# Optimization experiments

Hardware: AMD Instinct MI355X
Metric: run time of the kernel (lower is better)

## Reference

```python
import jax, jax.numpy as jnp
import numpy as np

N_HEAD = 12
HEAD_DIM = 64
N_EMBD = 768
ATTN_MULT = 0.125
B, T = 2, 2048
NEG_INF = -1e30


def setup_inputs() -> dict:
    key = jax.random.key(0)
    ks = jax.random.split(key, 3)
    x = jax.random.normal(ks[0], (B, T, N_EMBD), dtype=jnp.float32)
    W_attn = jax.random.normal(ks[1], (N_EMBD, 3 * N_HEAD * HEAD_DIM), dtype=jnp.float32) * 0.02
    b_attn = jnp.zeros((3 * N_HEAD * HEAD_DIM,), dtype=jnp.float32)
    W_proj = jax.random.normal(ks[2], (N_HEAD * HEAD_DIM, N_EMBD), dtype=jnp.float32) * 0.02
    b_proj = jnp.zeros((N_EMBD,), dtype=jnp.float32)
    return {"x": x, "W_attn": W_attn, "b_attn": b_attn, "W_proj": W_proj, "b_proj": b_proj}


def reference(x, W_attn, b_attn, W_proj, b_proj):
    Bsz, Tlen, C = x.shape
    H, D = N_HEAD, HEAD_DIM
    qkv = x @ W_attn + b_attn                       # [B,T,3*H*D]
    q, k, v = jnp.split(qkv, 3, axis=-1)
    q = q.reshape(Bsz, Tlen, H, D).transpose(0, 2, 1, 3)   # [B,H,T,D]
    k = k.reshape(Bsz, Tlen, H, D).transpose(0, 2, 1, 3)
    v = v.reshape(Bsz, Tlen, H, D).transpose(0, 2, 1, 3)

    att = jnp.einsum('bhtd,bhsd->bhts', q, k) * ATTN_MULT  # [B,H,T,T]
    causal = jnp.tril(jnp.ones((Tlen, Tlen), dtype=bool))  # [T,T]
    att = jnp.where(causal, att, NEG_INF)

    # selection mask from head 0 (SelectionHeadLinearComboKind.NONE)
    S = jax.nn.relu(att[:, 0:1, :, :])                     # [B,1,T,T]; relu kills -inf
    # protect_bos_token: zero column 0 (key index 0)
    col = jnp.arange(Tlen)
    S = S * (col[None, None, None, :] != 0)
    # prevent_from_masking_myself: zero diagonal
    S = S * (1.0 - jnp.eye(Tlen, dtype=S.dtype))

    # accumulate selection over query (row) axis: ProtectionKind.NONE
    FF = jnp.cumsum(S, axis=-2)                            # [B,1,T,T]
    att = att - FF                                         # broadcast over heads

    p = jax.nn.softmax(att, axis=-1)                       # [B,H,T,T]
    y = jnp.einsum('bhts,bhsd->bhtd', p, v)                # [B,H,T,D]
    y = y.transpose(0, 2, 1, 3).reshape(Bsz, Tlen, H * D)  # [B,T,H*D]
    return y @ W_proj + b_proj
```

## Files before the change

kernel.cpp:

```cpp
#include <hip/hip_runtime.h>
#include <math.h>

#define T 2048
#define NH 12
#define HD 64
#define C3 2304
#define CE 768
#define NB 2

typedef __attribute__((ext_vector_type(8))) short bf16x8;
typedef __attribute__((ext_vector_type(4))) float f32x4;

__device__ inline void bf16split(float a, unsigned short& h, unsigned short& l) {
    unsigned int u = __float_as_uint(a);
    unsigned int r = (u + 0x7FFFu + ((u >> 16) & 1u)) >> 16;
    h = (unsigned short)r;
    float hf = __uint_as_float(r << 16);
    float lo = a - hf;
    unsigned int v = __float_as_uint(lo);
    l = (unsigned short)((v + 0x7FFFu + ((v >> 16) & 1u)) >> 16);
}

__global__ __launch_bounds__(256) void cvt_split_kernel(const float* __restrict__ A,
        unsigned short* __restrict__ H, unsigned short* __restrict__ L) {
    int i = blockIdx.x * 256 + threadIdx.x;
    float4 a0 = *(reinterpret_cast<const float4*>(A) + (size_t)i * 2);
    float4 a1 = *(reinterpret_cast<const float4*>(A) + (size_t)i * 2 + 1);
    float f[8] = {a0.x, a0.y, a0.z, a0.w, a1.x, a1.y, a1.z, a1.w};
    unsigned short h[8], l[8];
    #pragma unroll
    for (int j = 0; j < 8; ++j) bf16split(f[j], h[j], l[j]);
    uint4 hv, lv;
    hv.x = (unsigned)h[0] | ((unsigned)h[1] << 16); hv.y = (unsigned)h[2] | ((unsigned)h[3] << 16);
    hv.z = (unsigned)h[4] | ((unsigned)h[5] << 16); hv.w = (unsigned)h[6] | ((unsigned)h[7] << 16);
    lv.x = (unsigned)l[0] | ((unsigned)l[1] << 16); lv.y = (unsigned)l[2] | ((unsigned)l[3] << 16);
    lv.z = (unsigned)l[4] | ((unsigned)l[5] << 16); lv.w = (unsigned)l[6] | ((unsigned)l[7] << 16);
    reinterpret_cast<uint4*>(H)[i] = hv;
    reinterpret_cast<uint4*>(L)[i] = lv;
}

__global__ __launch_bounds__(256) void cvt_split_T_kernel(const float* __restrict__ W,
        unsigned short* __restrict__ H, unsigned short* __restrict__ L, int K, int N) {
    __shared__ float tile[64][65];
    const int n0 = blockIdx.x * 64, k0 = blockIdx.y * 64;
    const int t = threadIdx.x;
    {
        int r = t >> 2, c4 = (t & 3) * 16;
        #pragma unroll
        for (int u = 0; u < 4; ++u) {
            float4 w = *reinterpret_cast<const float4*>(&W[(size_t)(k0 + r) * N + n0 + c4 + u * 4]);
            tile[r][c4 + u * 4 + 0] = w.x; tile[r][c4 + u * 4 + 1] = w.y;
            tile[r][c4 + u * 4 + 2] = w.z; tile[r][c4 + u * 4 + 3] = w.w;
        }
    }
    __syncthreads();
    {
        int n = t >> 2, kc = (t & 3) * 16;
        unsigned short h[16], l[16];
        #pragma unroll
        for (int j = 0; j < 16; ++j) bf16split(tile[kc + j][n], h[j], l[j]);
        uint4 hv0, hv1, lv0, lv1;
        hv0.x = (unsigned)h[0] | ((unsigned)h[1] << 16);  hv0.y = (unsigned)h[2] | ((unsigned)h[3] << 16);
        hv0.z = (unsigned)h[4] | ((unsigned)h[5] << 16);  hv0.w = (unsigned)h[6] | ((unsigned)h[7] << 16);
        hv1.x = (unsigned)h[8] | ((unsigned)h[9] << 16);  hv1.y = (unsigned)h[10] | ((unsigned)h[11] << 16);
        hv1.z = (unsigned)h[12] | ((unsigned)h[13] << 16); hv1.w = (unsigned)h[14] | ((unsigned)h[15] << 16);
        lv0.x = (unsigned)l[0] | ((unsigned)l[1] << 16);  lv0.y = (unsigned)l[2] | ((unsigned)l[3] << 16);
        lv0.z = (unsigned)l[4] | ((unsigned)l[5] << 16);  lv0.w = (unsigned)l[6] | ((unsigned)l[7] << 16);
        lv1.x = (unsigned)l[8] | ((unsigned)l[9] << 16);  lv1.y = (unsigned)l[10] | ((unsigned)l[11] << 16);
        lv1.z = (unsigned)l[12] | ((unsigned)l[13] << 16); lv1.w = (unsigned)l[14] | ((unsigned)l[15] << 16);
        size_t o = (size_t)(n0 + n) * K + k0 + kc;
        reinterpret_cast<uint4*>(&H[o])[0] = hv0; reinterpret_cast<uint4*>(&H[o])[1] = hv1;
        reinterpret_cast<uint4*>(&L[o])[0] = lv0; reinterpret_cast<uint4*>(&L[o])[1] = lv1;
    }
}

__global__ __launch_bounds__(256) void cvt_qk_kernel(const float* __restrict__ qkv,
        unsigned short* __restrict__ Qh, unsigned short* __restrict__ Ql,
        unsigned short* __restrict__ Kh, unsigned short* __restrict__ Kl) {
    int t = blockIdx.x * 256 + threadIdx.x;
    int dg = t & 7;
    int s = (t >> 3) & (T - 1);
    int bh = t >> 14;
    int b = bh / NH, h = bh % NH;
    const float* qs = qkv + (size_t)(b * T + s) * C3 + h * 64 + dg * 8;
    const float* ks = qs + 768;
    size_t o = ((size_t)bh * T + s) * 64 + dg * 8;
    #pragma unroll
    for (int which = 0; which < 2; ++which) {
        const float* src = (which == 0) ? qs : ks;
        float4 a0 = *reinterpret_cast<const float4*>(src);
        float4 a1 = *reinterpret_cast<const float4*>(src + 4);
        float f[8] = {a0.x, a0.y, a0.z, a0.w, a1.x, a1.y, a1.z, a1.w};
        unsigned short hh[8], ll[8];
        #pragma unroll
        for (int j = 0; j < 8; ++j) bf16split(f[j], hh[j], ll[j]);
        uint4 hv, lv;
        hv.x = (unsigned)hh[0] | ((unsigned)hh[1] << 16); hv.y = (unsigned)hh[2] | ((unsigned)hh[3] << 16);
        hv.z = (unsigned)hh[4] | ((unsigned)hh[5] << 16); hv.w = (unsigned)hh[6] | ((unsigned)hh[7] << 16);
        lv.x = (unsigned)ll[0] | ((unsigned)ll[1] << 16); lv.y = (unsigned)ll[2] | ((unsigned)ll[3] << 16);
        lv.z = (unsigned)ll[4] | ((unsigned)ll[5] << 16); lv.w = (unsigned)ll[6] | ((unsigned)ll[7] << 16);
        if (which == 0) {
            *reinterpret_cast<uint4*>(&Qh[o]) = hv;
            *reinterpret_cast<uint4*>(&Ql[o]) = lv;
// ... 245 lines not shown
        }
        return;
    }
    __shared__ float Qt[64][68];
    __shared__ float Kt[64][68];
    {
        int r = tid >> 2;
        int c0 = (tid & 3) * 16;
        const float* qrow = qkv + (size_t)(b * T + qb + r) * C3 + 0;
        const float* krow = qkv + (size_t)(b * T + kb + r) * C3 + 768;
        #pragma unroll
        for (int u = 0; u < 4; ++u) {
            float4 q4 = *reinterpret_cast<const float4*>(&qrow[c0 + u * 4]);
            float4 k4 = *reinterpret_cast<const float4*>(&krow[c0 + u * 4]);
            int d = c0 + u * 4;
            Qt[d + 0][r] = q4.x; Qt[d + 1][r] = q4.y; Qt[d + 2][r] = q4.z; Qt[d + 3][r] = q4.w;
            Kt[d + 0][r] = k4.x; Kt[d + 1][r] = k4.y; Kt[d + 2][r] = k4.z; Kt[d + 3][r] = k4.w;
        }
    }
    __syncthreads();
    float acc[4][4] = {};
    #pragma unroll
    for (int d = 0; d < 64; ++d) {
        float4 qv = *reinterpret_cast<const float4*>(&Qt[d][ty * 4]);
        float4 kv = *reinterpret_cast<const float4*>(&Kt[d][tx * 4]);
        float qa[4] = {qv.x, qv.y, qv.z, qv.w};
        float ka[4] = {kv.x, kv.y, kv.z, kv.w};
        #pragma unroll
        for (int i = 0; i < 4; ++i)
            #pragma unroll
            for (int j = 0; j < 4; ++j)
                acc[i][j] = fmaf(qa[i], ka[j], acc[i][j]);
    }
    #pragma unroll
    for (int i = 0; i < 4; ++i) {
        int t = qb + ty * 4 + i;
        float o[4];
        #pragma unroll
        for (int j = 0; j < 4; ++j) {
            int s = kb + tx * 4 + j;
            float v = acc[i][j] * 0.125f;
            o[j] = (s >= 1 && s < t) ? fmaxf(v, 0.0f) : 0.0f;
        }
        float4 o4 = {o[0], o[1], o[2], o[3]};
        *reinterpret_cast<float4*>(&Sb[(size_t)t * T + kb + tx * 4]) = o4;
    }
}

__global__ __launch_bounds__(256) void colsum_kernel(const float* __restrict__ S,
                                                     float* __restrict__ Psum) {
    int s = blockIdx.x * 256 + threadIdx.x;
    int j = blockIdx.y, b = blockIdx.z;
    const float* Sb = S + (size_t)b * T * T;
    float sum = 0.f;
    for (int r = 0; r < 64; ++r) sum += Sb[(size_t)(j * 64 + r) * T + s];
    Psum[((size_t)b * 32 + j) * T + s] = sum;
}

__global__ __launch_bounds__(256) void scanseg_kernel(float* __restrict__ Psum) {
    int s = blockIdx.x * 256 + threadIdx.x;
    int b = blockIdx.y;
    float run = 0.f;
    for (int j = 0; j < 32; ++j) {
        size_t idx = ((size_t)b * 32 + j) * T + s;
        float v = Psum[idx];
        Psum[idx] = run;
        run += v;
    }
}

__global__ __launch_bounds__(256) void ffscan_kernel(float* __restrict__ S,
                                                     const float* __restrict__ Psum) {
    int s = blockIdx.x * 256 + threadIdx.x;
    int j = blockIdx.y, b = blockIdx.z;
    float run = Psum[((size_t)b * 32 + j) * T + s];
    float* Sb = S + (size_t)b * T * T;
    for (int r = 0; r < 64; ++r) {
        size_t idx = (size_t)(j * 64 + r) * T + s;
        run += Sb[idx];
        Sb[idx] = run;
    }
}

__device__ inline int chunk_base_fn(int qt) {
    int base = 0;
    for (int q = 8; q < qt; ++q) base += (q + 8) >> 3;
    return base;
}

__global__ __launch_bounds__(256) void flash_mfma_kernel(
        const unsigned short* __restrict__ Qh, const unsigned short* __restrict__ Ql,
        const unsigned short* __restrict__ Kh, const unsigned short* __restrict__ Kl,
        const unsigned short* __restrict__ Vth, const unsigned short* __restrict__ Vtl,
        const float* __restrict__ FF, float* __restrict__ Y,
        float* __restrict__ PART) {
    const int hb = blockIdx.x;
    const int h = hb % NH, b = hb / NH;
    int qt = 0, kt0 = 0, kt1 = 1;
    {
        int u = blockIdx.y, cnt = 0;
        bool found = false;
        for (int sz = 8; sz >= 1 && !found; --sz) {
            for (int q = 31; q >= 0; --q) {
                int nch = (q + 8) >> 3;
                int nfull = nch - 1;
                int last = q + 1 - 8 * nfull;
                int nthis = ((sz == 8) ? nfull : 0) + ((last == sz) ? 1 : 0);
                if (u < cnt + nthis) {
                    int off = u - cnt;
                    qt = q;
                    int ci = (sz == 8 && off < nfull) ? off : nfull;
                    kt0 = ci * 8;
                    kt1 = (ci == nfull) ? (q + 1) : (kt0 + 8);
                    found = true;
                    break;
                }
                cnt += nthis;
            }
        }
    }
    const int qb = qt * 64;
    const int tid = threadIdx.x;
    const int lane = tid & 63, w = tid >> 6;
    const int fr = lane & 15, fg = lane >> 4;
    __shared__ unsigned short KP[2][64 * FST];
    __shared__ unsigned short Vt[2][64 * FST];

    bf16x8 qh[2], ql[2];
    #pragma unroll
    for (int ks = 0; ks < 2; ++ks) {
        size_t qo = ((size_t)hb * T + qb + w * 16 + fr) * 64 + ks * 32 + fg * 8;
        qh[ks] = *reinterpret_cast<const bf16x8*>(&Qh[qo]);
        ql[ks] = *reinterpret_cast<const bf16x8*>(&Ql[qo]);
    }

    float m[4], l[4];
    f32x4 Oacc[4];
    #pragma unroll
    for (int p = 0; p < 4; ++p) { m[p] = -1e30f; l[p] = 0.f; }
    #pragma unroll
    for (int fd = 0; fd < 4; ++fd) Oacc[fd] = (f32x4){0.f, 0.f, 0.f, 0.f};

    const float* FFb = FF + (size_t)b * T * T;
    const int sr = tid >> 2, sc0 = (tid & 3) * 16;

    for (int kt = kt0; kt < kt1; ++kt) {
        const int kb = kt * 64;
        __syncthreads();
        {
            const unsigned short* ksrc = Kh + ((size_t)hb * T + kb + sr) * 64 + sc0;
            const unsigned short* ksrl = Kl + ((size_t)hb * T + kb + sr) * 64 + sc0;
            const unsigned short* vsrc = Vth + ((size_t)hb * 64 + sr) * T + kb + sc0;
            const unsigned short* vsrl = Vtl + ((size_t)hb * 64 + sr) * T + kb + sc0;
            uint4 k0v = reinterpret_cast<const uint4*>(ksrc)[0];
            uint4 k1v = reinterpret_cast<const uint4*>(ksrc)[1];
            uint4 k2v = reinterpret_cast<const uint4*>(ksrl)[0];
            uint4 k3v = reinterpret_cast<const uint4*>(ksrl)[1];
            uint4 v0v = reinterpret_cast<const uint4*>(vsrc)[0];
            uint4 v1v = reinterpret_cast<const uint4*>(vsrc)[1];
            uint4 v2v = reinterpret_cast<const uint4*>(vsrl)[0];
            uint4 v3v = reinterpret_cast<const uint4*>(vsrl)[1];
            *reinterpret_cast<uint4*>(&KP[0][sr * FST + sc0 + 0]) = k0v;
            *reinterpret_cast<uint4*>(&KP[0][sr * FST + sc0 + 8]) = k1v;
            *reinterpret_cast<uint4*>(&KP[1][sr * FST + sc0 + 0]) = k2v;
            *reinterpret_cast<uint4*>(&KP[1][sr * FST + sc0 + 8]) = k3v;
            *reinterpret_cast<uint4*>(&Vt[0][sr * FST + sc0 + 0]) = v0v;
            *reinterpret_cast<uint4*>(&Vt[0][sr * FST + sc0 + 8]) = v1v;
            *reinterpret_cast<uint4*>(&Vt[1][sr * FST + sc0 + 0]) = v2v;
            *reinterpret_cast<uint4*>(&Vt[1][sr * FST + sc0 + 8]) = v3v;
        }
        __syncthreads();
        float ffv[4][4];
        #pragma unroll
        for (int p = 0; p < 4; ++p) {
            int t = qb + w * 16 + fg * 4 + p;
            #pragma unroll
            for (int fj = 0; fj < 4; ++fj)
                ffv[p][fj] = FFb[(size_t)t * T + kb + fj * 16 + fr];
        }
        f32x4 qk[4];
        #pragma unroll
        for (int fj = 0; fj < 4; ++fj) qk[fj] = (f32x4){0.f, 0.f, 0.f, 0.f};
        #pragma unroll
        for (int ks = 0; ks < 2; ++ks) {
            bf16x8 kbh[4], kbl[4];
            #pragma unroll
            for (int fj = 0; fj < 4; ++fj) {
                kbh[fj] = *reinterpret_cast<const bf16x8*>(&KP[0][(fj * 16 + fr) * FST + ks * 32 + fg * 8]);
                kbl[fj] = *reinterpret_cast<const bf16x8*>(&KP[1][(fj * 16 + fr) * FST + ks * 32 + fg * 8]);
            }
            #pragma unroll
            for (int fj = 0; fj < 4; ++fj) {
                qk[fj] = __builtin_amdgcn_mfma_f32_16x16x32_bf16(qh[ks], kbh[fj], qk[fj], 0, 0, 0);
                qk[fj] = __builtin_amdgcn_mfma_f32_16x16x32_bf16(qh[ks], kbl[fj], qk[fj], 0, 0, 0);
                qk[fj] = __builtin_amdgcn_mfma_f32_16x16x32_bf16(ql[ks], kbh[fj], qk[fj], 0, 0, 0);
            }
        }
        float sc[4][4];
        #pragma unroll
        for (int p = 0; p < 4; ++p) {
            int t = qb + w * 16 + fg * 4 + p;
            #pragma unroll
            for (int fj = 0; fj < 4; ++fj) {
                int s = kb + fj * 16 + fr;
                float v = qk[fj][p] * 0.125f - ffv[p][fj];
                sc[fj][p] = (s <= t) ? v : -1e30f;
            }
        }
        #pragma unroll
        for (int p = 0; p < 4; ++p) {
            float tm = fmaxf(fmaxf(sc[0][p], sc[1][p]), fmaxf(sc[2][p], sc[3][p]));
            tm = fmaxf(tm, __shfl_xor(tm, 1));
            tm = fmaxf(tm, __shfl_xor(tm, 2));
            tm = fmaxf(tm, __shfl_xor(tm, 4));
            tm = fmaxf(tm, __shfl_xor(tm, 8));
            float mn = fmaxf(m[p], tm);
            float scale = __expf(m[p] - mn);
            float rs = 0.f;
            #pragma unroll
            for (int fj = 0; fj < 4; ++fj) {
                float pe = __expf(sc[fj][p] - mn);
                sc[fj][p] = pe; rs += pe;
            }
            rs += __shfl_xor(rs, 1); rs += __shfl_xor(rs, 2);
            rs += __shfl_xor(rs, 4); rs += __shfl_xor(rs, 8);
            l[p] = l[p] * scale + rs;
            m[p] = mn;
            #pragma unroll
            for (int fd = 0; fd < 4; ++fd) Oacc[fd][p] *= scale;
        }
        __syncthreads();
        #pragma unroll
        for (int p = 0; p < 4; ++p) {
            int qrow = w * 16 + fg * 4 + p;
            #pragma unroll
            for (int fj = 0; fj < 4; ++fj) {
                unsigned short hh, ll;
                bf16split(sc[fj][p], hh, ll);
                KP[0][qrow * FST + fj * 16 + fr] = hh;
                KP[1][qrow * FST + fj * 16 + fr] = ll;
            }
        }
        __syncthreads();
        #pragma unroll
        for (int ks = 0; ks < 2; ++ks) {
            bf16x8 pah = *reinterpret_cast<const bf16x8*>(&KP[0][(w * 16 + fr) * FST + ks * 32 + fg * 8]);
            bf16x8 pal = *reinterpret_cast<const bf16x8*>(&KP[1][(w * 16 + fr) * FST + ks * 32 + fg * 8]);
            bf16x8 vbh[4], vbl[4];
            #pragma unroll
            for (int fd = 0; fd < 4; ++fd) {
                vbh[fd] = *reinterpret_cast<const bf16x8*>(&Vt[0][(fd * 16 + fr) * FST + ks * 32 + fg * 8]);
                vbl[fd] = *reinterpret_cast<const bf16x8*>(&Vt[1][(fd * 16 + fr) * FST + ks * 32 + fg * 8]);
            }
            #pragma unroll
            for (int fd = 0; fd < 4; ++fd) {
                Oacc[fd] = __builtin_amdgcn_mfma_f32_16x16x32_bf16(pah, vbh[fd], Oacc[fd], 0, 0, 0);
                Oacc[fd] = __builtin_amdgcn_mfma_f32_16x16x32_bf16(pah, vbl[fd], Oacc[fd], 0, 0, 0);
                Oacc[fd] = __builtin_amdgcn_mfma_f32_16x16x32_bf16(pal, vbh[fd], Oacc[fd], 0, 0, 0);
            }
        }
    }
    if (qt < 8) {
        #pragma unroll
        for (int p = 0; p < 4; ++p) {
            int t = qb + w * 16 + fg * 4 + p;
            float inv = 1.f / l[p];
            float* Yrow = Y + (size_t)(b * T + t) * CE + h * 64;
            #pragma unroll
            for (int fd = 0; fd < 4; ++fd)
                Yrow[fd * 16 + fr] = Oacc[fd][p] * inv;
        }
    } else {
        const int cb = chunk_base_fn(qt) + (kt0 >> 3);
        float* Ob = PART + (size_t)(hb * 72 + cb) * 4224;
        #pragma unroll
        for (int p = 0; p < 4; ++p) {
            int rr = w * 16 + fg * 4 + p;
            #pragma unroll
            for (int fd = 0; fd < 4; ++fd)
                Ob[rr * 64 + fd * 16 + fr] = Oacc[fd][p];
            if (fr == 0) { Ob[4096 + rr] = m[p]; Ob[4096 + 64 + rr] = l[p]; }
        }
    }
}

__global__ __launch_bounds__(256) void merge8_kernel(const float* __restrict__ PART,
                                                     float* __restrict__ Y) {
    const int hb = blockIdx.x;
    const int qt = 8 + blockIdx.y;
    const int h = hb % NH, b = hb / NH;
    const int nch = (qt + 8) >> 3;
    const float* base = PART + (size_t)(hb * 72 + chunk_base_fn(qt)) * 4224;
    const int tid = threadIdx.x;
    const int r = tid >> 2, c0 = (tid & 3) * 16;
    float mm[4], ll[4];
    float M = -1e30f;
    #pragma unroll
    for (int c = 0; c < 4; ++c) {
        int cc = (c < nch) ? c : 0;
        float mv = base[(size_t)cc * 4224 + 4096 + r];
        float lv = base[(size_t)cc * 4224 + 4096 + 64 + r];
        mm[c] = (c < nch) ? mv : -1e30f;
        ll[c] = (c < nch) ? lv : 0.f;
        M = fmaxf(M, mm[c]);
    }
    float a[4], L = 0.f;
    #pragma unroll
    for (int c = 0; c < 4; ++c) {
        a[c] = (c < nch) ? __expf(mm[c] - M) : 0.f;
        L += a[c] * ll[c];
    }
    float inv = 1.f / L;
    const int t = qt * 64 + r;
    float* Yrow = Y + (size_t)(b * T + t) * CE + h * 64;
    #pragma unroll
    for (int u = 0; u < 4; ++u) {
        float ax = 0.f, ay = 0.f, az = 0.f, aw = 0.f;
        #pragma unroll
        for (int c = 0; c < 4; ++c) {
            int cc = (c < nch) ? c : 0;
            float4 xo = *reinterpret_cast<const float4*>(&base[(size_t)cc * 4224 + r * 64 + c0 + u * 4]);
            ax += a[c] * xo.x; ay += a[c] * xo.y; az += a[c] * xo.z; aw += a[c] * xo.w;
        }
        float4 y = {ax * inv, ay * inv, az * inv, aw * inv};
        *reinterpret_cast<float4*>(&Yrow[c0 + u * 4]) = y;
    }
}

__global__ __launch_bounds__(256) void flash_kernel(const float* __restrict__ qkv,
                                                    const float* __restrict__ FF,
                                                    float* __restrict__ Y,
                                                    float* __restrict__ PO,
                                                    float* __restrict__ PML,
                                                    int split) {
    const int hb = blockIdx.x;
    const int h = hb % NH, b = hb / NH;
    int qt, kt0, kt1, mode;
    if (split) {
        const int u = blockIdx.y;
        if (u < 16)      { qt = 16 + u; kt0 = 0;  kt1 = 16;     mode = 1; }
        else if (u < 32) { qt = 31 - u; kt0 = 0;  kt1 = qt + 1; mode = 0; }
        else             { qt = 63 - u; kt0 = 16; kt1 = qt + 1; mode = 2; }
    } else {
        qt = 31 - blockIdx.y; kt0 = 0; kt1 = qt + 1; mode = 0;
    }
    const int qb = qt * 64;
    const int tid = threadIdx.x, ty = tid >> 4, tx = tid & 15;
    __shared__ float Qt[64][68];
    __shared__ float KtPs[64][68];
    __shared__ float Vs[64][68];
    const int r = tid >> 2, c0 = (tid & 3) * 16;
    {
        const float* qrow = qkv + (size_t)(b * T + qb + r) * C3 + h * 64;
        #pragma unroll
        for (int u = 0; u < 4; ++u) {
            float4 q4 = *reinterpret_cast<const float4*>(&qrow[c0 + u * 4]);
            int d = c0 + u * 4;
            Qt[d + 0][r] = q4.x; Qt[d + 1][r] = q4.y; Qt[d + 2][r] = q4.z; Qt[d + 3][r] = q4.w;
        }
    }
    float m[4], l[4], O[4][4];
    #pragma unroll
    for (int i = 0; i < 4; ++i) {
        m[i] = -1e30f; l[i] = 0.f;
        #pragma unroll
        for (int j = 0; j < 4; ++j) O[i][j] = 0.f;
    }
    const float* FFb = FF + (size_t)b * T * T;
    for (int kt = kt0; kt < kt1; ++kt) {
        const int kb = kt * 64;
        __syncthreads();
        {
            const float* krow = qkv + (size_t)(b * T + kb + r) * C3 + 768 + h * 64;
            const float* vrow = qkv + (size_t)(b * T + kb + r) * C3 + 1536 + h * 64;
            #pragma unroll
            for (int u = 0; u < 4; ++u) {
                float4 k4 = *reinterpret_cast<const float4*>(&krow[c0 + u * 4]);
                int d = c0 + u * 4;
                KtPs[d + 0][r] = k4.x; KtPs[d + 1][r] = k4.y;
                KtPs[d + 2][r] = k4.z; KtPs[d + 3][r] = k4.w;
                *reinterpret_cast<float4*>(&Vs[r][c0 + u * 4]) =
                    *reinterpret_cast<const float4*>(&vrow[c0 + u * 4]);
            }
        }
        __syncthreads();
        float sc[4][4] = {};
        #pragma unroll
        for (int d = 0; d < 64; ++d) {
            float4 qv = *reinterpret_cast<const float4*>(&Qt[d][ty * 4]);
            float4 kv = *reinterpret_cast<const float4*>(&KtPs[d][tx * 4]);
            float qa[4] = {qv.x, qv.y, qv.z, qv.w};
            float ka[4] = {kv.x, kv.y, kv.z, kv.w};
            #pragma unroll
            for (int i = 0; i < 4; ++i)
                #pragma unroll
                for (int j = 0; j < 4; ++j)
                    sc[i][j] = fmaf(qa[i], ka[j], sc[i][j]);
        }
        #pragma unroll
        for (int i = 0; i < 4; ++i) {
            int t = qb + ty * 4 + i;
            float4 f4 = *reinterpret_cast<const float4*>(&FFb[(size_t)t * T + kb + tx * 4]);
            float fv[4] = {f4.x, f4.y, f4.z, f4.w};
            #pragma unroll
            for (int j = 0; j < 4; ++j) {
                int s = kb + tx * 4 + j;
                float v = sc[i][j] * 0.125f - fv[j];
                sc[i][j] = (s <= t) ? v : -1e30f;
            }
        }
        #pragma unroll
        for (int i = 0; i < 4; ++i) {
            float tm = fmaxf(fmaxf(sc[i][0], sc[i][1]), fmaxf(sc[i][2], sc[i][3]));
            tm = fmaxf(tm, __shfl_xor(tm, 1));
            tm = fmaxf(tm, __shfl_xor(tm, 2));
            tm = fmaxf(tm, __shfl_xor(tm, 4));
            tm = fmaxf(tm, __shfl_xor(tm, 8));
            float mn = fmaxf(m[i], tm);
            float scale = __expf(m[i] - mn);
            float rs = 0.f;
            #pragma unroll
            for (int j = 0; j < 4; ++j) {
                float p = __expf(sc[i][j] - mn);
                sc[i][j] = p; rs += p;
            }
            rs += __shfl_xor(rs, 1); rs += __shfl_xor(rs, 2);
            rs += __shfl_xor(rs, 4); rs += __shfl_xor(rs, 8);
            l[i] = l[i] * scale + rs;
            m[i] = mn;
            #pragma unroll
            for (int j = 0; j < 4; ++j) O[i][j] *= scale;
        }
        __syncthreads();
        #pragma unroll
        for (int i = 0; i < 4; ++i) {
            float4 p4 = {sc[i][0], sc[i][1], sc[i][2], sc[i][3]};
            *reinterpret_cast<float4*>(&KtPs[ty * 4 + i][tx * 4]) = p4;
        }
        __syncthreads();
        #pragma unroll
        for (int j4 = 0; j4 < 16; ++j4) {
            float pv[4][4];
            #pragma unroll
            for (int i = 0; i < 4; ++i) {
                float4 t4 = *reinterpret_cast<const float4*>(&KtPs[ty * 4 + i][j4 * 4]);
                pv[i][0] = t4.x; pv[i][1] = t4.y; pv[i][2] = t4.z; pv[i][3] = t4.w;
            }
            #pragma unroll
            for (int jj = 0; jj < 4; ++jj) {
                float4 v4 = *reinterpret_cast<const float4*>(&Vs[j4 * 4 + jj][tx * 4]);
                float vv[4] = {v4.x, v4.y, v4.z, v4.w};
                #pragma unroll
                for (int i = 0; i < 4; ++i)
                    #pragma unroll
                    for (int dd = 0; dd < 4; ++dd)
                        O[i][dd] = fmaf(pv[i][jj], vv[dd], O[i][dd]);
            }
        }
    }
    if (mode == 0) {
        #pragma unroll
        for (int i = 0; i < 4; ++i) {
            int t = qb + ty * 4 + i;
            float inv = 1.f / l[i];
            float4 o4 = {O[i][0] * inv, O[i][1] * inv, O[i][2] * inv, O[i][3] * inv};
            *reinterpret_cast<float4*>(&Y[(size_t)(b * T + t) * CE + h * 64 + tx * 4]) = o4;
        }
    } else {
        const int pidx = (b * NH + h) * 16 + (qt - 16);
        float* Ob  = PO  + (size_t)(mode - 1) * (NB * NH * 16 * 4096) + (size_t)pidx * 4096;
        float* mlb = PML + (size_t)(mode - 1) * (NB * NH * 16 * 128)  + (size_t)pidx * 128;
        #pragma unroll
        for (int i = 0; i < 4; ++i) {
            int rr = ty * 4 + i;
            float4 o4 = {O[i][0], O[i][1], O[i][2], O[i][3]};
            *reinterpret_cast<float4*>(&Ob[rr * 64 + tx * 4]) = o4;
            if (tx == 0) { mlb[rr] = m[i]; mlb[64 + rr] = l[i]; }
        }
    }
}

__global__ __launch_bounds__(256) void merge_kernel(const float* __restrict__ PO,
                                                    const float* __restrict__ PML,
                                                    float* __restrict__ Y) {
    const int p = blockIdx.x;
    const int q16 = p & 15;
    const int hb = p >> 4;
    const int h = hb % NH, b = hb / NH;
    const int qt = 16 + q16;
    const float* O0  = PO  + (size_t)p * 4096;
    const float* O1  = PO  + (size_t)(NB * NH * 16) * 4096 + (size_t)p * 4096;
    const float* ml0 = PML + (size_t)p * 128;
    const float* ml1 = PML + (size_t)(NB * NH * 16) * 128  + (size_t)p * 128;
    const int tid = threadIdx.x;
    const int r = tid >> 2, c0 = (tid & 3) * 16;
    float m0 = ml0[r], l0 = ml0[64 + r];
    float m1 = ml1[r], l1 = ml1[64 + r];
    float M  = fmaxf(m0, m1);
    float a0 = __expf(m0 - M), a1 = __expf(m1 - M);
    float inv = 1.f / (a0 * l0 + a1 * l1);
    const int t = qt * 64 + r;
    float* Yrow = Y + (size_t)(b * T + t) * CE + h * 64;
    #pragma unroll
    for (int u = 0; u < 4; ++u) {
        float4 x0 = *reinterpret_cast<const float4*>(&O0[r * 64 + c0 + u * 4]);
        float4 x1 = *reinterpret_cast<const float4*>(&O1[r * 64 + c0 + u * 4]);
        float4 y;
        y.x = (a0 * x0.x + a1 * x1.x) * inv;
        y.y = (a0 * x0.y + a1 * x1.y) * inv;
        y.z = (a0 * x0.z + a1 * x1.z) * inv;
        y.w = (a0 * x0.w + a1 * x1.w) * inv;
        *reinterpret_cast<float4*>(&Yrow[c0 + u * 4]) = y;
    }
}

extern "C" void kernel_launch(void* const* d_in, const int* in_sizes, int n_in,
                              void* d_out, int out_size, void* d_ws, size_t ws_size,
                              hipStream_t stream) {
    const float* x      = (const float*)d_in[0];
    const float* W_attn = (const float*)d_in[1];
    const float* b_attn = (const float*)d_in[2];
    const float* W_proj = (const float*)d_in[3];
    const float* b_proj = (const float*)d_in[4];
    float* out = (float*)d_out;

    char* ws = (char*)d_ws;
    const size_t QKV_BYTES = (size_t)NB * T * C3 * 4;
    const size_t S_BYTES   = (size_t)NB * T * T * 4;
    const size_t P_BYTES   = (size_t)NB * 32 * T * 4;
    const size_t Y_BYTES   = (size_t)NB * T * CE * 4;
    const size_t PO_BYTES  = (size_t)2 * NB * NH * 16 * 4096 * 4;
    const size_t PML_BYTES = (size_t)2 * NB * NH * 16 * 128 * 4;
    const size_t PLANE_X   = (size_t)NB * T * CE * 2;
    const size_t PLANE_WA  = (size_t)C3 * CE * 2;
    const size_t PLANE_WP  = (size_t)CE * CE * 2;
    const size_t PLANE_KV  = (size_t)NB * NH * T * 64 * 2;

    const size_t U_OFF  = QKV_BYTES + S_BYTES + P_BYTES + Y_BYTES;
    const size_t U_SIZE = PO_BYTES + PML_BYTES;
    const size_t W_OFF  = U_OFF + U_SIZE;
    const size_t KV_OFF = W_OFF + 2 * PLANE_WA + 2 * PLANE_WP;

    float* qkv  = (float*)ws;
    float* S    = (float*)(ws + QKV_BYTES);
    float* Psum = (float*)(ws + QKV_BYTES + S_BYTES);
    float* Yb   = (float*)(ws + QKV_BYTES + S_BYTES + P_BYTES);
    float* PO   = (float*)(ws + U_OFF);
    float* PML  = (float*)(ws + U_OFF + PO_BYTES);
    unsigned short* Xh  = (unsigned short*)(ws + U_OFF);
    unsigned short* Xl  = (unsigned short*)(ws + U_OFF + PLANE_X);
    unsigned short* Qhp = Xh;
    unsigned short* Qlp = Xl;
    unsigned short* Yh  = Xh;
    unsigned short* Yl  = Xl;
    unsigned short* WAh = (unsigned short*)(ws + W_OFF);
    unsigned short* WAl = (unsigned short*)(ws + W_OFF + PLANE_WA);
    unsigned short* WPh = (unsigned short*)(ws + W_OFF + 2 * PLANE_WA);
    unsigned short* WPl = (unsigned short*)(ws + W_OFF + 2 * PLANE_WA + PLANE_WP);
    unsigned short* Khp = (unsigned short*)(ws + KV_OFF);
    unsigned short* Klp = (unsigned short*)(ws + KV_OFF + PLANE_KV);
    unsigned short* VTh = (unsigned short*)(ws + KV_OFF + 2 * PLANE_KV);
    unsigned short* VTl = (unsigned short*)(ws + KV_OFF + 3 * PLANE_KV);
    float* PART = qkv;

    const size_t NEED_SPLIT = U_OFF + U_SIZE;
    const size_t NEED_MFMA  = KV_OFF;
    const size_t NEED_KV    = KV_OFF + 4 * PLANE_KV;
    const int split = (ws_size >= NEED_SPLIT) ? 1 : 0;
    const int mfma  = (ws_size >= NEED_MFMA) ? 1 : 0;
    const int kv    = (ws_size >= NEED_KV && mfma) ? 1 : 0;

    const int M = NB * T;

    if (mfma) {
        cvt_split_T_kernel<<<dim3(C3 / 64, CE / 64), 256, 0, stream>>>(W_attn, WAh, WAl, CE, C3);
        cvt_split_T_kernel<<<dim3(CE / 64, CE / 64), 256, 0, stream>>>(W_proj, WPh, WPl, CE, CE);
        cvt_split_kernel<<<dim3((M * CE / 8) / 256), 256, 0, stream>>>(x, Xh, Xl);
        gemm_mfma_kernel<<<dim3(C3 / 128, M / 128), 256, 0, stream>>>(Xh, Xl, WAh, WAl, b_attn, qkv, M, C3, CE);
    } else {
        gemm_bias_kernel<<<dim3(C3 / 64, M / 64), 256, 0, stream>>>(x, W_attn, b_attn, qkv, M, C3, CE);
    }
    if (kv) {
        cvt_qk_kernel<<<dim3((NB * NH * T * 8) / 256), 256, 0, stream>>>(qkv, Qhp, Qlp, Khp, Klp);
        cvt_kv_vt_kernel<<<dim3(T / 64, NB * NH), 256, 0, stream>>>(qkv, VTh, VTl);
        s0_mfma_kernel<<<dim3(T / 64, T / 64, NB), 256, 0, stream>>>(Qhp, Qlp, Khp, Klp, S);
    } else {
        s0_kernel<<<dim3(T / 64, T / 64, NB), 256, 0, stream>>>(qkv, S);
    }
    colsum_kernel<<<dim3(T / 256, 32, NB), 256, 0, stream>>>(S, Psum);
    scanseg_kernel<<<dim3(T / 256, NB), 256, 0, stream>>>(Psum);
    ffscan_kernel<<<dim3(T / 256, 32, NB), 256, 0, stream>>>(S, Psum);
    if (kv) {
        flash_mfma_kernel<<<dim3(NB * NH, 80), 256, 0, stream>>>(Qhp, Qlp, Khp, Klp, VTh, VTl, S, Yb, PART);
        merge8_kernel<<<dim3(NB * NH, 24), 256, 0, stream>>>(PART, Yb);
    } else if (split) {
        flash_kernel<<<dim3(NB * NH, 48), 256, 0, stream>>>(qkv, S, Yb, PO, PML, 1);
        merge_kernel<<<dim3(NB * NH * 16), 256, 0, stream>>>(PO, PML, Yb);
    } else {
        flash_kernel<<<dim3(NB * NH, 32), 256, 0, stream>>>(qkv, S, Yb, PO, PML, 0);
    }
    if (mfma) {
        cvt_split_kernel<<<dim3((M * CE / 8) / 256), 256, 0, stream>>>(Yb, Yh, Yl);
        gemm_mfma_kernel<<<dim3(CE / 128, M / 128), 256, 0, stream>>>(Yh, Yl, WPh, WPl, b_proj, out, M, CE, CE);
    } else {
        gemm_bias_kernel<<<dim3(CE / 64, M / 64), 256, 0, stream>>>(Yb, W_proj, b_proj, out, M, CE, CE);
    }
}
```

Before: 296.5 us.

## Use 128-row query tiles with 32x32 MFMA and register-resident P in flash kernel

Restructures the flash attention kernel to process 128-query tiles using 32x32x16 bf16 MFMAs, where each wave owns 32 query rows. Scores are computed transposed so the softmax row stats need only a single cross-half shuffle. P is repacked through lane shuffles instead of a round trip through shared memory, which removes two barriers per key tile. Work partitioning moves to precomputed lookup tables with 40 blocks and a matching 128-row merge kernel. Fewer, larger blocks reuse K/V more but may lower occupancy and raise register pressure.

```diff
diff --git a/kernel.cpp b/kernel.cpp
--- a/kernel.cpp
+++ b/kernel.cpp
@@ -10,6 +10,8 @@
 
 typedef __attribute__((ext_vector_type(8))) short bf16x8;
 typedef __attribute__((ext_vector_type(4))) float f32x4;
+typedef __attribute__((ext_vector_type(16))) float f32x16;
+typedef __attribute__((ext_vector_type(4))) unsigned u32x4;
 
 __device__ inline void bf16split(float a, unsigned short& h, unsigned short& l) {
     unsigned int u = __float_as_uint(a);
@@ -19,6 +21,13 @@
     float lo = a - hf;
     unsigned int v = __float_as_uint(lo);
     l = (unsigned short)((v + 0x7FFFu + ((v >> 16) & 1u)) >> 16);
+}
+
+__device__ inline void packP(float a, float b, unsigned& wh, unsigned& wl) {
+    unsigned short ha, la, hb, lb;
+    bf16split(a, ha, la); bf16split(b, hb, lb);
+    wh = (unsigned)ha | ((unsigned)hb << 16);
+    wl = (unsigned)la | ((unsigned)lb << 16);
 }
 
 __global__ __launch_bounds__(256) void cvt_split_kernel(const float* __restrict__ A,
@@ -430,11 +439,10 @@
     }
 }
 
-__device__ inline int chunk_base_fn(int qt) {
-    int base = 0;
-    for (int q = 8; q < qt; ++q) base += (q + 8) >> 3;
-    return base;
-}
+__device__ const int FTQ[40] = {15,15,15,15,14,14,14,13,13,13,12,12,12,11,11,11,10,10,9,9,8,8,7,7,6,5,4,3,14,10,6,2,13,9,5,1,12,8,4,0};
+__device__ const int FK0[40] = {0,8,16,24,0,8,16,0,8,16,0,8,16,0,8,16,0,8,0,8,0,8,0,8,0,0,0,0,24,16,8,0,24,16,8,0,24,16,8,0};
+__device__ const int FK1[40] = {8,16,24,32,8,16,24,8,16,24,8,16,24,8,16,24,8,16,8,16,8,16,8,16,8,8,8,8,30,22,14,6,28,20,12,4,26,18,10,2};
+__device__ const int FCB[12] = {0,2,4,6,8,11,14,17,20,24,28,32};
 
 __global__ __launch_bounds__(256) void flash_mfma_kernel(
         const unsigned short* __restrict__ Qh, const unsigned short* __restrict__ Ql,
@@ -444,51 +452,26 @@
         float* __restrict__ PART) {
     const int hb = blockIdx.x;
     const int h = hb % NH, b = hb / NH;
-    int qt = 0, kt0 = 0, kt1 = 1;
-    {
-        int u = blockIdx.y, cnt = 0;
-        bool found = false;
-        for (int sz = 8; sz >= 1 && !found; --sz) {
-            for (int q = 31; q >= 0; --q) {
-                int nch = (q + 8) >> 3;
-                int nfull = nch - 1;
-                int last = q + 1 - 8 * nfull;
-                int nthis = ((sz == 8) ? nfull : 0) + ((last == sz) ? 1 : 0);
-                if (u < cnt + nthis) {
-                    int off = u - cnt;
-                    qt = q;
-                    int ci = (sz == 8 && off < nfull) ? off : nfull;
-                    kt0 = ci * 8;
-                    kt1 = (ci == nfull) ? (q + 1) : (kt0 + 8);
-                    found = true;
-                    break;
-                }
-                cnt += nthis;
-            }
-        }
-    }
-    const int qb = qt * 64;
+    const int u = blockIdx.y;
+    const int tq = FTQ[u], kt0 = FK0[u], kt1 = FK1[u];
+    const int qb = tq * 128;
     const int tid = threadIdx.x;
     const int lane = tid & 63, w = tid >> 6;
-    const int fr = lane & 15, fg = lane >> 4;
-    __shared__ unsigned short KP[2][64 * FST];
-    __shared__ unsigned short Vt[2][64 * FST];
-
-    bf16x8 qh[2], ql[2];
-    #pragma unroll
-    for (int ks = 0; ks < 2; ++ks) {
-        size_t qo = ((size_t)hb * T + qb + w * 16 + fr) * 64 + ks * 32 + fg * 8;
-        qh[ks] = *reinterpret_cast<const bf16x8*>(&Qh[qo]);
-        ql[ks] = *reinterpret_cast<const bf16x8*>(&Ql[qo]);
-    }
-
-    float m[4], l[4];
-    f32x4 Oacc[4];
-    #pragma unroll
-    for (int p = 0; p < 4; ++p) { m[p] = -1e30f; l[p] = 0.f; }
-    #pragma unroll
-    for (int fd = 0; fd < 4; ++fd) Oacc[fd] = (f32x4){0.f, 0.f, 0.f, 0.f};
-
+    const int q31 = lane & 31, hi = lane >> 5;
+    const int trow = qb + w * 32 + q31;
+    __shared__ unsigned short KS[2][64 * FST];
+    __shared__ unsigned short VS[2][64 * FST];
+
+    bf16x8 qfh[4], qfl[4];
+    #pragma unroll
+    for (int dblk = 0; dblk < 4; ++dblk) {
+        size_t qo = ((size_t)hb * T + trow) * 64 + dblk * 16 + hi * 8;
+        qfh[dblk] = *reinterpret_cast<const bf16x8*>(&Qh[qo]);
+        qfl[dblk] = *reinterpret_cast<const bf16x8*>(&Ql[qo]);
+    }
+
+    f32x16 oacc0 = (f32x16)(0.f), oacc1 = (f32x16)(0.f);
+    float m = -1e30f, l = 0.f;
     const float* FFb = FF + (size_t)b * T * T;
     const int sr = tid >> 2, sc0 = (tid & 3) * 16;
 
@@ -508,170 +491,182 @@
             uint4 v1v = reinterpret_cast<const uint4*>(vsrc)[1];
             uint4 v2v = reinterpret_cast<const uint4*>(vsrl)[0];
             uint4 v3v = reinterpret_cast<const uint4*>(vsrl)[1];
-            *reinterpret_cast<uint4*>(&KP[0][sr * FST + sc0 + 0]) = k0v;
-            *reinterpret_cast<uint4*>(&KP[0][sr * FST + sc0 + 8]) = k1v;
-            *reinterpret_cast<uint4*>(&KP[1][sr * FST + sc0 + 0]) = k2v;
-            *reinterpret_cast<uint4*>(&KP[1][sr * FST + sc0 + 8]) = k3v;
-            *reinterpret_cast<uint4*>(&Vt[0][sr * FST + sc0 + 0]) = v0v;
-            *reinterpret_cast<uint4*>(&Vt[0][sr * FST + sc0 + 8]) = v1v;
-            *reinterpret_cast<uint4*>(&Vt[1][sr * FST + sc0 + 0]) = v2v;
-            *reinterpret_cast<uint4*>(&Vt[1][sr * FST + sc0 + 8]) = v3v;
+            *reinterpret_cast<uint4*>(&KS[0][sr * FST + sc0 + 0]) = k0v;
+            *reinterpret_cast<uint4*>(&KS[0][sr * FST + sc0 + 8]) = k1v;
+            *reinterpret_cast<uint4*>(&KS[1][sr * FST + sc0 + 0]) = k2v;
+            *reinterpret_cast<uint4*>(&KS[1][sr * FST + sc0 + 8]) = k3v;
+            *reinterpret_cast<uint4*>(&VS[0][sr * FST + sc0 + 0]) = v0v;
+            *reinterpret_cast<uint4*>(&VS[0][sr * FST + sc0 + 8]) = v1v;
+            *reinterpret_cast<uint4*>(&VS[1][sr * FST + sc0 + 0]) = v2v;
+            *reinterpret_cast<uint4*>(&VS[1][sr * FST + sc0 + 8]) = v3v;
         }
         __syncthreads();
-        float ffv[4][4];
-        #pragma unroll
-        for (int p = 0; p < 4; ++p) {
-            int t = qb + w * 16 + fg * 4 + p;
-            #pragma unroll
-            for (int fj = 0; fj < 4; ++fj)
-                ffv[p][fj] = FFb[(size_t)t * T + kb + fj * 16 + fr];
-        }
-        f32x4 qk[4];
-        #pragma unroll
-        for (int fj = 0; fj < 4; ++fj) qk[fj] = (f32x4){0.f, 0.f, 0.f, 0.f};
-        #pragma unroll
-        for (int ks = 0; ks < 2; ++ks) {
-            bf16x8 kbh[4], kbl[4];
-            #pragma unroll
-            for (int fj = 0; fj < 4; ++fj) {
-                kbh[fj] = *reinterpret_cast<const bf16x8*>(&KP[0][(fj * 16 + fr) * FST + ks * 32 + fg * 8]);
-                kbl[fj] = *reinterpret_cast<const bf16x8*>(&KP[1][(fj * 16 + fr) * FST + ks * 32 + fg * 8]);
-            }
-            #pragma unroll
-            for (int fj = 0; fj < 4; ++fj) {
-                qk[fj] = __builtin_amdgcn_mfma_f32_16x16x32_bf16(qh[ks], kbh[fj], qk[fj], 0, 0, 0);
-                qk[fj] = __builtin_amdgcn_mfma_f32_16x16x32_bf16(qh[ks], kbl[fj], qk[fj], 0, 0, 0);
-                qk[fj] = __builtin_amdgcn_mfma_f32_16x16x32_bf16(ql[ks], kbh[fj], qk[fj], 0, 0, 0);
-            }
-        }
-        float sc[4][4];
-        #pragma unroll
-        for (int p = 0; p < 4; ++p) {
-            int t = qb + w * 16 + fg * 4 + p;
-            #pragma unroll
-            for (int fj = 0; fj < 4; ++fj) {
-                int s = kb + fj * 16 + fr;
-                float v = qk[fj][p] * 0.125f - ffv[p][fj];
-                sc[fj][p] = (s <= t) ? v : -1e30f;
-            }
-        }
-        #pragma unroll
-        for (int p = 0; p < 4; ++p) {
-            float tm = fmaxf(fmaxf(sc[0][p], sc[1][p]), fmaxf(sc[2][p], sc[3][p]));
-            tm = fmaxf(tm, __shfl_xor(tm, 1));
-            tm = fmaxf(tm, __shfl_xor(tm, 2));
-            tm = fmaxf(tm, __shfl_xor(tm, 4));
-            tm = fmaxf(tm, __shfl_xor(tm, 8));
-            float mn = fmaxf(m[p], tm);
-            float scale = __expf(m[p] - mn);
-            float rs = 0.f;
-            #pragma unroll
-            for (int fj = 0; fj < 4; ++fj) {
-                float pe = __expf(sc[fj][p] - mn);
-                sc[fj][p] = pe; rs += pe;
-            }
-            rs += __shfl_xor(rs, 1); rs += __shfl_xor(rs, 2);
-            rs += __shfl_xor(rs, 4); rs += __shfl_xor(rs, 8);
-            l[p] = l[p] * scale + rs;
-            m[p] = mn;
-            #pragma unroll
-            for (int fd = 0; fd < 4; ++fd) Oacc[fd][p] *= scale;
-        }
-        __syncthreads();
-        #pragma unroll
-        for (int p = 0; p < 4; ++p) {
-            int qrow = w * 16 + fg * 4 + p;
-            #pragma unroll
-            for (int fj = 0; fj < 4; ++fj) {
-                unsigned short hh, ll;
-                bf16split(sc[fj][p], hh, ll);
-                KP[0][qrow * FST + fj * 16 + fr] = hh;
-                KP[1][qrow * FST + fj * 16 + fr] = ll;
-            }
-        }
-        __syncthreads();
-        #pragma unroll
-        for (int ks = 0; ks < 2; ++ks) {
-            bf16x8 pah = *reinterpret_cast<const bf16x8*>(&KP[0][(w * 16 + fr) * FST + ks * 32 + fg * 8]);
-            bf16x8 pal = *reinterpret_cast<const bf16x8*>(&KP[1][(w * 16 + fr) * FST + ks * 32 + fg * 8]);
-            bf16x8 vbh[4], vbl[4];
-            #pragma unroll
-            for (int fd = 0; fd < 4; ++fd) {
-                vbh[fd] = *reinterpret_cast<const bf16x8*>(&Vt[0][(fd * 16 + fr) * FST + ks * 32 + fg * 8]);
-                vbl[fd] = *reinterpret_cast<const bf16x8*>(&Vt[1][(fd * 16 + fr) * FST + ks * 32 + fg * 8]);
-            }
-            #pragma unroll
-            for (int fd = 0; fd < 4; ++fd) {
-                Oacc[fd] = __builtin_amdgcn_mfma_f32_16x16x32_bf16(pah, vbh[fd], Oacc[fd], 0, 0, 0);
-                Oacc[fd] = __builtin_amdgcn_mfma_f32_16x16x32_bf16(pah, vbl[fd], Oacc[fd], 0, 0, 0);
-                Oacc[fd] = __builtin_amdgcn_mfma_f32_16x16x32_bf16(pal, vbh[fd], Oacc[fd], 0, 0, 0);
-            }
-        }
-    }
-    if (qt < 8) {
-        #pragma unroll
-        for (int p = 0; p < 4; ++p) {
-            int t = qb + w * 16 + fg * 4 + p;
-            float inv = 1.f / l[p];
-            float* Yrow = Y + (size_t)(b * T + t) * CE + h * 64;
-            #pragma unroll
-            for (int fd = 0; fd < 4; ++fd)
-                Yrow[fd * 16 + fr] = Oacc[fd][p] * inv;
+        f32x16 acc[2];
+        acc[0] = (f32x16)(0.f); acc[1] = (f32x16)(0.f);
+        #pragma unroll
+        for (int sb = 0; sb < 2; ++sb) {
+            #pragma unroll
+            for (int dblk = 0; dblk < 4; ++dblk) {
+                bf16x8 kfh = *reinterpret_cast<const bf16x8*>(&KS[0][(sb * 32 + q31) * FST + dblk * 16 + hi * 8]);
+                bf16x8 kfl = *reinterpret_cast<const bf16x8*>(&KS[1][(sb * 32 + q31) * FST + dblk * 16 + hi * 8]);
+                acc[sb] = __builtin_amdgcn_mfma_f32_32x32x16_bf16(kfh, qfh[dblk], acc[sb], 0, 0, 0);
+                acc[sb] = __builtin_amdgcn_mfma_f32_32x32x16_bf16(kfh, qfl[dblk], acc[sb], 0, 0, 0);
+                acc[sb] = __builtin_amdgcn_mfma_f32_32x32x16_bf16(kfl, qfh[dblk], acc[sb], 0, 0, 0);
+            }
+        }
+        float pv[2][16];
+        #pragma unroll
+        for (int sb = 0; sb < 2; ++sb) {
+            #pragma unroll
+            for (int g = 0; g < 4; ++g) {
+                float4 f4 = *reinterpret_cast<const float4*>(
+                    &FFb[(size_t)trow * T + kb + sb * 32 + g * 8 + hi * 4]);
+                float fv[4] = {f4.x, f4.y, f4.z, f4.w};
+                #pragma unroll
+                for (int a = 0; a < 4; ++a) {
+                    int r = g * 4 + a;
+                    int s = kb + sb * 32 + a + g * 8 + hi * 4;
+                    float val = acc[sb][r] * 0.125f - fv[a];
+                    pv[sb][r] = (s <= trow) ? val : -1e30f;
+                }
+            }
+        }
+        float tm = pv[0][0];
+        #pragma unroll
+        for (int sb = 0; sb < 2; ++sb)
+            #pragma unroll
+            for (int r = 0; r < 16; ++r) tm = fmaxf(tm, pv[sb][r]);
+        tm = fmaxf(tm, __shfl_xor(tm, 32));
+        float mn = fmaxf(m, tm);
+        float scale = __expf(m - mn);
+        float rs = 0.f;
+        #pragma unroll
+        for (int sb = 0; sb < 2; ++sb)
+            #pragma unroll
+            for (int r = 0; r < 16; ++r) {
+                float pe = __expf(pv[sb][r] - mn);
+                pv[sb][r] = pe; rs += pe;
+            }
+        rs += __shfl_xor(rs, 32);
+        l = l * scale + rs;
+        m = mn;
+        oacc0 *= scale; oacc1 *= scale;
+        unsigned wh[2][4][2], wl[2][4][2];
+        #pragma unroll
+        for (int sb = 0; sb < 2; ++sb)
+            #pragma unroll
+            for (int bq = 0; bq < 4; ++bq)
+                #pragma unroll
+                for (int h2 = 0; h2 < 2; ++h2)
+                    packP(pv[sb][4 * bq + 2 * h2], pv[sb][4 * bq + 2 * h2 + 1],
+                          wh[sb][bq][h2], wl[sb][bq][h2]);
+        #pragma unroll
+        for (int kk = 0; kk < 4; ++kk) {
+            const int sb = kk >> 1;
+            const int b0 = 2 * (kk & 1), b1 = b0 + 1;
+            unsigned sh_b1_0 = (unsigned)__shfl_xor((int)wh[sb][b1][0], 32);
+            unsigned sh_b1_1 = (unsigned)__shfl_xor((int)wh[sb][b1][1], 32);
+            unsigned sh_b0_0 = (unsigned)__shfl_xor((int)wh[sb][b0][0], 32);
+            unsigned sh_b0_1 = (unsigned)__shfl_xor((int)wh[sb][b0][1], 32);
+            unsigned sl_b1_0 = (unsigned)__shfl_xor((int)wl[sb][b1][0], 32);
+            unsigned sl_b1_1 = (unsigned)__shfl_xor((int)wl[sb][b1][1], 32);
+            unsigned sl_b0_0 = (unsigned)__shfl_xor((int)wl[sb][b0][0], 32);
+            unsigned sl_b0_1 = (unsigned)__shfl_xor((int)wl[sb][b0][1], 32);
+            u32x4 th, tl;
+            th[0] = hi ? sh_b1_0 : wh[sb][b0][0];
+            th[1] = hi ? sh_b1_1 : wh[sb][b0][1];
+            th[2] = hi ? wh[sb][b1][0] : sh_b0_0;
+            th[3] = hi ? wh[sb][b1][1] : sh_b0_1;
+            tl[0] = hi ? sl_b1_0 : wl[sb][b0][0];
+            tl[1] = hi ? sl_b1_1 : wl[sb][b0][1];
+            tl[2] = hi ? wl[sb][b1][0] : sl_b0_0;
+            tl[3] = hi ? wl[sb][b1][1] : sl_b0_1;
+            bf16x8 pbh = __builtin_bit_cast(bf16x8, th);
+            bf16x8 pbl = __builtin_bit_cast(bf16x8, tl);
+            {
+                bf16x8 vfh = *reinterpret_cast<const bf16x8*>(&VS[0][(q31) * FST + kk * 16 + hi * 8]);
+                bf16x8 vfl = *reinterpret_cast<const bf16x8*>(&VS[1][(q31) * FST + kk * 16 + hi * 8]);
+                oacc0 = __builtin_amdgcn_mfma_f32_32x32x16_bf16(vfh, pbh, oacc0, 0, 0, 0);
+                oacc0 = __builtin_amdgcn_mfma_f32_32x32x16_bf16(vfh, pbl, oacc0, 0, 0, 0);
+                oacc0 = __builtin_amdgcn_mfma_f32_32x32x16_bf16(vfl, pbh, oacc0, 0, 0, 0);
+            }
+            {
+                bf16x8 vfh = *reinterpret_cast<const bf16x8*>(&VS[0][(32 + q31) * FST + kk * 16 + hi * 8]);
+                bf16x8 vfl = *reinterpret_cast<const bf16x8*>(&VS[1][(32 + q31) * FST + kk * 16 + hi * 8]);
+                oacc1 = __builtin_amdgcn_mfma_f32_32x32x16_bf16(vfh, pbh, oacc1, 0, 0, 0);
+                oacc1 = __builtin_amdgcn_mfma_f32_32x32x16_bf16(vfh, pbl, oacc1, 0, 0, 0);
+                oacc1 = __builtin_amdgcn_mfma_f32_32x32x16_bf16(vfl, pbh, oacc1, 0, 0, 0);
+            }
+        }
+    }
+    if (tq < 4) {
+        float inv = 1.f / l;
+        float* Yrow = Y + (size_t)(b * T + trow) * CE + h * 64;
+        #pragma unroll
+        for (int g = 0; g < 4; ++g) {
+            float4 o0 = {oacc0[4 * g + 0] * inv, oacc0[4 * g + 1] * inv,
+                         oacc0[4 * g + 2] * inv, oacc0[4 * g + 3] * inv};
+            float4 o1 = {oacc1[4 * g + 0] * inv, oacc1[4 * g + 1] * inv,
+                         oacc1[4 * g + 2] * inv, oacc1[4 * g + 3] * inv};
+            *reinterpret_cast<float4*>(&Yrow[g * 8 + hi * 4]) = o0;
+            *reinterpret_cast<float4*>(&Yrow[32 + g * 8 + hi * 4]) = o1;
         }
     } else {
-        const int cb = chunk_base_fn(qt) + (kt0 >> 3);
-        float* Ob = PART + (size_t)(hb * 72 + cb) * 4224;
-        #pragma unroll
-        for (int p = 0; p < 4; ++p) {
-            int rr = w * 16 + fg * 4 + p;
-            #pragma unroll
-            for (int fd = 0; fd < 4; ++fd)
-                Ob[rr * 64 + fd * 16 + fr] = Oacc[fd][p];
-            if (fr == 0) { Ob[4096 + rr] = m[p]; Ob[4096 + 64 + rr] = l[p]; }
-        }
-    }
-}
-
-__global__ __launch_bounds__(256) void merge8_kernel(const float* __restrict__ PART,
-                                                     float* __restrict__ Y) {
+        const int ci = FCB[tq - 4] + (kt0 >> 3);
+        float* Ob = PART + (size_t)(hb * 36 + ci) * 8448;
+        const int rr = w * 32 + q31;
+        #pragma unroll
+        for (int g = 0; g < 4; ++g) {
+            float4 o0 = {oacc0[4 * g + 0], oacc0[4 * g + 1], oacc0[4 * g + 2], oacc0[4 * g + 3]};
+            float4 o1 = {oacc1[4 * g + 0], oacc1[4 * g + 1], oacc1[4 * g + 2], oacc1[4 * g + 3]};
+            *reinterpret_cast<float4*>(&Ob[rr * 64 + g * 8 + hi * 4]) = o0;
+            *reinterpret_cast<float4*>(&Ob[rr * 64 + 32 + g * 8 + hi * 4]) = o1;
+        }
+        if (hi == 0) { Ob[8192 + rr] = m; Ob[8192 + 128 + rr] = l; }
+    }
+}
+
+__global__ __launch_bounds__(256) void merge128_kernel(const float* __restrict__ PART,
+                                                       float* __restrict__ Y) {
     const int hb = blockIdx.x;
-    const int qt = 8 + blockIdx.y;
+    const int tq = 4 + blockIdx.y;
     const int h = hb % NH, b = hb / NH;
-    const int nch = (qt + 8) >> 3;
-    const float* base = PART + (size_t)(hb * 72 + chunk_base_fn(qt)) * 4224;
+    const int nch = (tq >= 12) ? 4 : (tq >= 8) ? 3 : 2;
+    const float* base = PART + (size_t)(hb * 36 + FCB[tq - 4]) * 8448;
     const int tid = threadIdx.x;
-    const int r = tid >> 2, c0 = (tid & 3) * 16;
-    float mm[4], ll[4];
+    const int r = tid >> 1, half = tid & 1;
+    float mm[4], la[4];
     float M = -1e30f;
     #pragma unroll
     for (int c = 0; c < 4; ++c) {
         int cc = (c < nch) ? c : 0;
-        float mv = base[(size_t)cc * 4224 + 4096 + r];
-        float lv = base[(size_t)cc * 4224 + 4096 + 64 + r];
+        float mv = base[(size_t)cc * 8448 + 8192 + r];
+        float lv = base[(size_t)cc * 8448 + 8192 + 128 + r];
         mm[c] = (c < nch) ? mv : -1e30f;
-        ll[c] = (c < nch) ? lv : 0.f;
+        la[c] = (c < nch) ? lv : 0.f;
         M = fmaxf(M, mm[c]);
     }
     float a[4], L = 0.f;
     #pragma unroll
     for (int c = 0; c < 4; ++c) {
         a[c] = (c < nch) ? __expf(mm[c] - M) : 0.f;
-        L += a[c] * ll[c];
+        L += a[c] * la[c];
     }
     float inv = 1.f / L;
-    const int t = qt * 64 + r;
-    float* Yrow = Y + (size_t)(b * T + t) * CE + h * 64;
-    #pragma unroll
-    for (int u = 0; u < 4; ++u) {
+    const int t = tq * 128 + r;
+    float* Yrow = Y + (size_t)(b * T + t) * CE + h * 64 + half * 32;
+    #pragma unroll
+    for (int uu = 0; uu < 8; ++uu) {
         float ax = 0.f, ay = 0.f, az = 0.f, aw = 0.f;
         #pragma unroll
         for (int c = 0; c < 4; ++c) {
             int cc = (c < nch) ? c : 0;
-            float4 xo = *reinterpret_cast<const float4*>(&base[(size_t)cc * 4224 + r * 64 + c0 + u * 4]);
-            ax += a[c] * xo.x; ay += a[c] * xo.y; az += a[c] * xo.z; aw += a[c] * xo.w;
+            float4 x = *reinterpret_cast<const float4*>(
+                &base[(size_t)cc * 8448 + r * 64 + half * 32 + uu * 4]);
+            ax += a[c] * x.x; ay += a[c] * x.y; az += a[c] * x.z; aw += a[c] * x.w;
         }
         float4 y = {ax * inv, ay * inv, az * inv, aw * inv};
-        *reinterpret_cast<float4*>(&Yrow[c0 + u * 4]) = y;
+        *reinterpret_cast<float4*>(&Yrow[uu * 4]) = y;
     }
 }
 
@@ -788,11 +783,11 @@
         __syncthreads();
         #pragma unroll
         for (int j4 = 0; j4 < 16; ++j4) {
-            float pv[4][4];
+            float pvv[4][4];
             #pragma unroll
             for (int i = 0; i < 4; ++i) {
                 float4 t4 = *reinterpret_cast<const float4*>(&KtPs[ty * 4 + i][j4 * 4]);
-                pv[i][0] = t4.x; pv[i][1] = t4.y; pv[i][2] = t4.z; pv[i][3] = t4.w;
+                pvv[i][0] = t4.x; pvv[i][1] = t4.y; pvv[i][2] = t4.z; pvv[i][3] = t4.w;
             }
             #pragma unroll
             for (int jj = 0; jj < 4; ++jj) {
@@ -802,7 +797,7 @@
                 for (int i = 0; i < 4; ++i)
                     #pragma unroll
                     for (int dd = 0; dd < 4; ++dd)
-                        O[i][dd] = fmaf(pv[i][jj], vv[dd], O[i][dd]);
+                        O[i][dd] = fmaf(pvv[i][jj], vv[dd], O[i][dd]);
             }
         }
     }
@@ -939,8 +934,8 @@
     scanseg_kernel<<<dim3(T / 256, NB), 256, 0, stream>>>(Psum);
     ffscan_kernel<<<dim3(T / 256, 32, NB), 256, 0, stream>>>(S, Psum);
     if (kv) {
-        flash_mfma_kernel<<<dim3(NB * NH, 80), 256, 0, stream>>>(Qhp, Qlp, Khp, Klp, VTh, VTl, S, Yb, PART);
-        merge8_kernel<<<dim3(NB * NH, 24), 256, 0, stream>>>(PART, Yb);
+        flash_mfma_kernel<<<dim3(NB * NH, 40), 256, 0, stream>>>(Qhp, Qlp, Khp, Klp, VTh, VTl, S, Yb, PART);
+        merge128_kernel<<<dim3(NB * NH, 12), 256, 0, stream>>>(PART, Yb);
     } else if (split) {
         flash_kernel<<<dim3(NB * NH, 48), 256, 0, stream>>>(qkv, S, Yb, PO, PML, 1);
         merge_kernel<<<dim3(NB * NH * 16), 256, 0, stream>>>(PO, PML, Yb);
```

After: 260.5 us. -12.1%, faster.
